# Performance work log

Hardware: AMD Instinct MI355X
Metric: run time of the kernel (lower is better)

The kernel has to match this reference:

```python
import jax, jax.numpy as jnp
import numpy as np

B, T, C, H = 4, 2048, 768, 64

def setup_inputs() -> dict:
    key = jax.random.key(0)
    kx, kq, kk, kv = jax.random.split(key, 4)
    x = jax.random.normal(kx, (B, T, C), dtype=jnp.float32)
    # torch Linear(C->H, bias=False): y = x @ W with W [C, H]
    s = 1.0 / np.sqrt(C)
    Wq = jax.random.normal(kq, (C, H), dtype=jnp.float32) * s
    Wk = jax.random.normal(kk, (C, H), dtype=jnp.float32) * s
    Wv = jax.random.normal(kv, (C, H), dtype=jnp.float32) * s
    return {"x": x, "Wq": Wq, "Wk": Wk, "Wv": Wv}

def reference(x, Wq, Wk, Wv):
    Bx, Tx, Cx = x.shape
    q = jnp.einsum('btc,ch->bth', x, Wq)
    k = jnp.einsum('btc,ch->bth', x, Wk)
    v = jnp.einsum('btc,ch->bth', x, Wv)
    # NOTE: original scales by C**-0.5 (n_embeddings), not head_size**-0.5
    w = jnp.einsum('bqh,bkh->bqk', q, k) * (Cx ** -0.5)  # [B, T, T]
    causal = jnp.tril(jnp.ones((Tx, Tx), dtype=bool))
    w = jnp.where(causal, w, -jnp.inf)
    w = jax.nn.softmax(w, axis=-1)
    # dropout: eval mode (identity)
    out = jnp.einsum('bqk,bkh->bqh', w, v)  # [B, T, H]
    return out
```

## Files before the change

### kernel.cpp

```cpp
#include <hip/hip_runtime.h>
#include <math.h>

#define TB 2048
#define CB 768
#define NB 4
#define NROWS (NB * TB)
#define NSMAX 16
#define WGPB 272

typedef __attribute__((ext_vector_type(8))) short bf16x8;
typedef __attribute__((ext_vector_type(4))) float f32x4;
typedef __attribute__((ext_vector_type(2))) float f32x2;
typedef __attribute__((ext_vector_type(2))) unsigned int u32x2;
typedef __attribute__((ext_vector_type(4))) unsigned int u32x4;

__device__ inline unsigned short f2bf(float f) {
  union { float f; unsigned u; } v; v.f = f;
  unsigned r = v.u + 0x7FFFu + ((v.u >> 16) & 1u);
  return (unsigned short)(r >> 16);
}
__device__ inline unsigned pack2bf(float a, float b) {
  return (unsigned)f2bf(a) | ((unsigned)f2bf(b) << 16);
}
__device__ inline float bf2f(unsigned short u) {
  union { unsigned u; float f; } v; v.u = (unsigned)u << 16; return v.f;
}
__device__ inline int groupP(int g) {
  int m = g >> 1;
  return (g & 1) ? (m + 1) * (m + 1) : m * (m + 1);
}

__global__ void cvt_w_kernel(const float* __restrict__ Wq, const float* __restrict__ Wk,
                             const float* __restrict__ Wv, unsigned short* __restrict__ Wt) {
  __shared__ float tw[64][65];
  const float* W = (blockIdx.y == 0) ? Wq : (blockIdx.y == 1) ? Wk : Wv;
  const int c0 = blockIdx.x * 64;
  const int row = threadIdx.x >> 2, seg = threadIdx.x & 3;
#pragma unroll
  for (int i = 0; i < 4; ++i) {
    float4 f = *(const float4*)(W + (size_t)(c0 + row) * 64 + seg * 16 + i * 4);
    tw[row][seg * 16 + i * 4 + 0] = f.x;
    tw[row][seg * 16 + i * 4 + 1] = f.y;
    tw[row][seg * 16 + i * 4 + 2] = f.z;
    tw[row][seg * 16 + i * 4 + 3] = f.w;
  }
  __syncthreads();
  const int j = threadIdx.x >> 2, cq = threadIdx.x & 3;
  unsigned short* dst = Wt + (size_t)(blockIdx.y * 64 + j) * CB + c0 + cq * 16;
  u32x4 ua, ub;
#pragma unroll
  for (int i = 0; i < 4; ++i) ua[i] = pack2bf(tw[cq * 16 + 2 * i][j], tw[cq * 16 + 2 * i + 1][j]);
#pragma unroll
  for (int i = 0; i < 4; ++i) ub[i] = pack2bf(tw[cq * 16 + 8 + 2 * i][j], tw[cq * 16 + 9 + 2 * i][j]);
  *(u32x4*)dst = ua;
  *(u32x4*)(dst + 8) = ub;
}

__launch_bounds__(256)
__global__ void proj_direct_kernel(const float* __restrict__ x,
                                   const unsigned short* __restrict__ Wt,
                                   unsigned short* __restrict__ q,
                                   unsigned short* __restrict__ k,
                                   unsigned short* __restrict__ vT) {
  __shared__ __align__(16) unsigned short xs[16 * 64];
  __shared__ float tr[64][17];
  const int tid = threadIdx.x;
  const int wv = tid >> 6;
  const int l = tid & 63;
  const int lrow = l & 15, lg = l >> 4;
  const int m0 = blockIdx.x * 16;
  const int srow = tid >> 4;
  const int sq = tid & 15;
  const float* xp = x + (size_t)(m0 + srow) * CB + sq * 4;
  const int swz = (srow & 7) << 4;

  f32x4 acc[3];
#pragma unroll
  for (int n = 0; n < 3; ++n) acc[n] = (f32x4){0.f, 0.f, 0.f, 0.f};

  float4 f = *(const float4*)xp;
  for (int k0 = 0; k0 < CB; k0 += 64) {
    {
      u32x2 c;
      c.x = pack2bf(f.x, f.y);
      c.y = pack2bf(f.z, f.w);
      *(u32x2*)((char*)xs + srow * 128 + ((sq * 8) ^ swz)) = c;
    }
    if (k0 + 64 < CB) f = *(const float4*)(xp + k0 + 64);
    __syncthreads();

#pragma unroll
    for (int s = 0; s < 2; ++s) {
      bf16x8 af = *(const bf16x8*)((const char*)xs + lrow * 128 +
                                   ((s * 64 + lg * 16) ^ ((lrow & 7) << 4)));
#pragma unroll
      for (int nf = 0; nf < 3; ++nf) {
        int col = wv * 48 + nf * 16 + lrow;
        bf16x8 bfr = *(const bf16x8*)(Wt + (size_t)col * CB + k0 + s * 32 + lg * 8);
        acc[nf] = __builtin_amdgcn_mfma_f32_16x16x32_bf16(af, bfr, acc[nf], 0, 0, 0);
      }
    }
    __syncthreads();
  }

#pragma unroll
  for (int nf = 0; nf < 3; ++nf) {
    int j = wv * 48 + nf * 16 + lrow;
#pragma unroll
    for (int r = 0; r < 4; ++r) {
      int grow = m0 + lg * 4 + r;
      if (j < 64)       q[(size_t)grow * 64 + j] = f2bf(acc[nf][r]);
      else if (j < 128) k[(size_t)grow * 64 + (j - 64)] = f2bf(acc[nf][r]);
      else              tr[j - 128][lg * 4 + r] = acc[nf][r];
    }
  }
  __syncthreads();
  {
    const int b = m0 >> 11, t0 = m0 & (TB - 1);
    const int h = tid >> 2, tq = tid & 3;
    u32x2 pk;
    pk.x = pack2bf(tr[h][tq * 4 + 0], tr[h][tq * 4 + 1]);
    pk.y = pack2bf(tr[h][tq * 4 + 2], tr[h][tq * 4 + 3]);
    *(u32x2*)(vT + ((size_t)(b * 64 + h)) * TB + t0 + tq * 4) = pk;
  }
}

__launch_bounds__(256)
__global__ void attn_kernel(const unsigned short* __restrict__ q,
                            const unsigned short* __restrict__ k,
                            const unsigned short* __restrict__ vT,
                            unsigned short* __restrict__ PO, float* __restrict__ Mp,
                            float* __restrict__ Lp) {
  __shared__ __align__(16) char ksm[2][8192];
  __shared__ __align__(16) char vsm[2][8192];
  const int tid = threadIdx.x;
  const int wid = tid >> 6, l = tid & 63;
  const int lrow = l & 15, lg = l >> 4;
  const int b = blockIdx.y;
  const int w = blockIdx.x;

  int g = (int)(2.f * sqrtf((float)w));
  if (g > 31) g = 31;
  while (g < 31 && groupP(g + 1) <= w) ++g;
  while (g > 0 && groupP(g) > w) --g;
  const int b128 = w - groupP(g);
  const int s64a = 2 * b128, s64b = 2 * b128 + 1;
  const bool has1 = (s64b <= g);
  const int kv0a = s64a * 64, kv0b = s64b * 64;
  const int qrow = (4 * g + wid) * 16 + lrow;

  const unsigned short* qb = q + (size_t)b * TB * 64;
  const char* kbb = (const char*)(k + (size_t)b * TB * 64);
  const unsigned short* vb = vT + (size_t)b * 64 * TB;

  const int srow = tid >> 2;
  const int sc = (tid & 3) * 32;
  const int kswz_w = (srow & 7) << 4;
  const int vswz_w = (srow & 3) << 5;

  float4 ka0 = *(const float4*)(kbb + (size_t)kv0a * 128 + tid * 32);
  float4 ka1 = *(const float4*)(kbb + (size_t)kv0a * 128 + tid * 32 + 16);
  const char* vrowa = (const char*)(vb + (size_t)srow * TB + kv0a);
  float4 va0 = *(const float4*)(vrowa + sc);
  float4 va1 = *(const float4*)(vrowa + sc + 16);

  bf16x8 qf[2];
#pragma unroll
  for (int s = 0; s < 2; ++s)
    qf[s] = *(const bf16x8*)(qb + (size_t)qrow * 64 + s * 32 + lg * 8);

  *(float4*)(ksm[0] + srow * 128 + ((sc + 0) ^ kswz_w)) = ka0;
  *(float4*)(ksm[0] + srow * 128 + ((sc + 16) ^ kswz_w)) = ka1;
  *(float4*)(vsm[0] + srow * 128 + ((sc + 0) ^ vswz_w)) = va0;
  *(float4*)(vsm[0] + srow * 128 + ((sc + 16) ^ vswz_w)) = va1;

  if (has1) {
    float4 kb0 = *(const float4*)(kbb + (size_t)kv0b * 128 + tid * 32);
    float4 kb1 = *(const float4*)(kbb + (size_t)kv0b * 128 + tid * 32 + 16);
    const char* vrowb = (const char*)(vb + (size_t)srow * TB + kv0b);
    float4 vb0 = *(const float4*)(vrowb + sc);
    float4 vb1 = *(const float4*)(vrowb + sc + 16);
    *(float4*)(ksm[1] + srow * 128 + ((sc + 0) ^ kswz_w)) = kb0;
    *(float4*)(ksm[1] + srow * 128 + ((sc + 16) ^ kswz_w)) = kb1;
    *(float4*)(vsm[1] + srow * 128 + ((sc + 0) ^ vswz_w)) = vb0;
    *(float4*)(vsm[1] + srow * 128 + ((sc + 16) ^ vswz_w)) = vb1;
  }
  __syncthreads();

  const int kswz = (lrow & 7) << 4;
  const float scale = 0.03608439182435161f;

  f32x4 S0[4];
#pragma unroll
  for (int cf = 0; cf < 4; ++cf) S0[cf] = (f32x4){0.f, 0.f, 0.f, 0.f};
#pragma unroll
  for (int cf = 0; cf < 4; ++cf) {
    const char* kp = ksm[0] + (cf * 16 + lrow) * 128;
#pragma unroll
    for (int s = 0; s < 2; ++s) {
      bf16x8 kf = *(const bf16x8*)(kp + ((s * 64 + lg * 16) ^ kswz));
      S0[cf] = __builtin_amdgcn_mfma_f32_16x16x32_bf16(kf, qf[s], S0[cf], 0, 0, 0);
    }
  }
  float tmx = -INFINITY;
  {
    const bool msk = (s64a == g);
#pragma unroll
    for (int cf = 0; cf < 4; ++cf)
#pragma unroll
      for (int r = 0; r < 4; ++r) {
        float vv = S0[cf][r] * scale;
        if (msk) {
          int kvi = kv0a + cf * 16 + lg * 4 + r;
          vv = (kvi > qrow) ? -INFINITY : vv;
        }
        S0[cf][r] = vv;
        tmx = fmaxf(tmx, vv);
      }
  }
  f32x4 S1[4];
  if (has1) {
#pragma unroll
    for (int cf = 0; cf < 4; ++cf) S1[cf] = (f32x4){0.f, 0.f, 0.f, 0.f};
#pragma unroll
    for (int cf = 0; cf < 4; ++cf) {
      const char* kp = ksm[1] + (cf * 16 + lrow) * 128;
#pragma unroll
      for (int s = 0; s < 2; ++s) {
        bf16x8 kf = *(const bf16x8*)(kp + ((s * 64 + lg * 16) ^ kswz));
        S1[cf] = __builtin_amdgcn_mfma_f32_16x16x32_bf16(kf, qf[s], S1[cf], 0, 0, 0);
      }
    }
    const bool msk = (s64b == g);
#pragma unroll
    for (int cf = 0; cf < 4; ++cf)
#pragma unroll
      for (int r = 0; r < 4; ++r) {
        float vv = S1[cf][r] * scale;
        if (msk) {
          int kvi = kv0b + cf * 16 + lg * 4 + r;
          vv = (kvi > qrow) ? -INFINITY : vv;
        }
        S1[cf][r] = vv;
        tmx = fmaxf(tmx, vv);
      }
  }
  tmx = fmaxf(tmx, __shfl_xor(tmx, 16));
  tmx = fmaxf(tmx, __shfl_xor(tmx, 32));

  float lsl = 0.f;
  f32x4 o[4];
#pragma unroll
  for (int hf = 0; hf < 4; ++hf) o[hf] = (f32x4){0.f, 0.f, 0.f, 0.f};
  const int rswz = (lrow & 3) << 5;

  {
    float p[4][4];
#pragma unroll
    for (int cf = 0; cf < 4; ++cf)
#pragma unroll
      for (int r = 0; r < 4; ++r) {
        float pe = __expf(S0[cf][r] - tmx);
        p[cf][r] = pe;
        lsl += pe;
      }
    union { unsigned u[4]; bf16x8 v; } pbu[2];
#pragma unroll
    for (int s = 0; s < 2; ++s) {
      pbu[s].u[0] = pack2bf(p[2 * s][0], p[2 * s][1]);
      pbu[s].u[1] = pack2bf(p[2 * s][2], p[2 * s][3]);
      pbu[s].u[2] = pack2bf(p[2 * s + 1][0], p[2 * s + 1][1]);
      pbu[s].u[3] = pack2bf(p[2 * s + 1][2], p[2 * s + 1][3]);
    }
#pragma unroll
    for (int s = 0; s < 2; ++s)
#pragma unroll
      for (int hf = 0; hf < 4; ++hf) {
        int r = hf * 16 + lrow;
        int a1 = r * 128 + ((s * 64 + lg * 8) ^ rswz);
        u32x2 lo = *(const u32x2*)(vsm[0] + a1);
        u32x2 hi = *(const u32x2*)(vsm[0] + (a1 ^ 32));
        union { unsigned u[4]; bf16x8 v; } vfu;
        vfu.u[0] = lo.x; vfu.u[1] = lo.y; vfu.u[2] = hi.x; vfu.u[3] = hi.y;
        o[hf] = __builtin_amdgcn_mfma_f32_16x16x32_bf16(vfu.v, pbu[s].v, o[hf], 0, 0, 0);
      }
  }
  if (has1) {
    float p[4][4];
#pragma unroll
    for (int cf = 0; cf < 4; ++cf)
#pragma unroll
      for (int r = 0; r < 4; ++r) {
        float pe = __expf(S1[cf][r] - tmx);
        p[cf][r] = pe;
        lsl += pe;
      }
    union { unsigned u[4]; bf16x8 v; } pbu[2];
#pragma unroll
    for (int s = 0; s < 2; ++s) {
      pbu[s].u[0] = pack2bf(p[2 * s][0], p[2 * s][1]);
      pbu[s].u[1] = pack2bf(p[2 * s][2], p[2 * s][3]);
      pbu[s].u[2] = pack2bf(p[2 * s + 1][0], p[2 * s + 1][1]);
      pbu[s].u[3] = pack2bf(p[2 * s + 1][2], p[2 * s + 1][3]);
    }
#pragma unroll
    for (int s = 0; s < 2; ++s)
#pragma unroll
      for (int hf = 0; hf < 4; ++hf) {
        int r = hf * 16 + lrow;
        int a1 = r * 128 + ((s * 64 + lg * 8) ^ rswz);
        u32x2 lo = *(const u32x2*)(vsm[1] + a1);
        u32x2 hi = *(const u32x2*)(vsm[1] + (a1 ^ 32));
        union { unsigned u[4]; bf16x8 v; } vfu;
        vfu.u[0] = lo.x; vfu.u[1] = lo.y; vfu.u[2] = hi.x; vfu.u[3] = hi.y;
        o[hf] = __builtin_amdgcn_mfma_f32_16x16x32_bf16(vfu.v, pbu[s].v, o[hf], 0, 0, 0);
      }
  }

  float ls = lsl;
  ls += __shfl_xor(ls, 16);
  ls += __shfl_xor(ls, 32);

  size_t rowg = (size_t)b128 * NROWS + b * TB + qrow;
  unsigned short* pop = PO + rowg * 64 + lg * 4;
#pragma unroll
  for (int hf = 0; hf < 4; ++hf) {
    u32x2 pk;
    pk.x = pack2bf(o[hf][0], o[hf][1]);
    pk.y = pack2bf(o[hf][2], o[hf][3]);
    *(u32x2*)(pop + hf * 16) = pk;
  }
  if (lg == 0) {
    Mp[rowg] = tmx;
    Lp[rowg] = ls;
  }
}

__global__ void attn_reduce_kernel(const unsigned short* __restrict__ PO,
                                   const float* __restrict__ Mp,
                                   const float* __restrict__ Lp,
                                   float* __restrict__ out) {
  int id = blockIdx.x * 256 + threadIdx.x;
  if (id >= NROWS * 32) return;
  int row = id >> 5, h0 = (id & 31) * 2;
  int t = row & (TB - 1);
  int ns = (t >> 7) + 1;
  float M = -INFINITY;
#pragma unroll 4
  for (int s = 0; s < ns; ++s) M = fmaxf(M, Mp[(size_t)s * NROWS + row]);
  float L = 0.f, a0 = 0.f, a1 = 0.f;
#pragma unroll 4
  for (int s = 0; s < ns; ++s) {
    float w = __expf(Mp[(size_t)s * NROWS + row] - M);
    L += Lp[(size_t)s * NROWS + row] * w;
    unsigned pv = *(const unsigned*)(PO + ((size_t)s * NROWS + row) * 64 + h0);
    a0 += bf2f((unsigned short)(pv & 0xffff)) * w;
    a1 += bf2f((unsigned short)(pv >> 16)) * w;
  }
  float rL = 1.f / L;
  f32x2 r; r.x = a0 * rL; r.y = a1 * rL;
  *(f32x2*)(out + (size_t)row * 64 + h0) = r;
}

extern "C" void kernel_launch(void* const* d_in, const int* in_sizes, int n_in,
                              void* d_out, int out_size, void* d_ws, size_t ws_size,
                              hipStream_t stream) {
  const float* x  = (const float*)d_in[0];
  const float* Wq = (const float*)d_in[1];
  const float* Wk = (const float*)d_in[2];
  const float* Wv = (const float*)d_in[3];
  float* out = (float*)d_out;

  unsigned short* Wt = (unsigned short*)d_ws;
  unsigned short* qb = Wt + 192 * CB;
  unsigned short* kb = qb + (size_t)NROWS * 64;
  unsigned short* vT = kb + (size_t)NROWS * 64;
  char* scratch = (char*)(vT + (size_t)NROWS * 64);

  unsigned short* PO = (unsigned short*)scratch;
  float* Mp = (float*)(scratch + (size_t)NSMAX * NROWS * 64 * 2);
  float* Lp = Mp + (size_t)NSMAX * NROWS;

  hipLaunchKernelGGL(cvt_w_kernel, dim3(12, 3), dim3(256), 0, stream,
                     Wq, Wk, Wv, Wt);
  hipLaunchKernelGGL(proj_direct_kernel, dim3(NROWS / 16), dim3(256), 0, stream,
                     x, Wt, qb, kb, vT);
  hipLaunchKernelGGL(attn_kernel, dim3(WGPB, NB), dim3(256), 0, stream,
                     qb, kb, vT, PO, Mp, Lp);
  hipLaunchKernelGGL(attn_reduce_kernel, dim3((NROWS * 32) / 256), dim3(256), 0, stream,
                     PO, Mp, Lp, out);
}
```

Baseline: 51.07 us.

## Widen attention workgroups to 128 query rows over full 128-key tiles

The attention kernel now runs 512-thread workgroups of 8 waves, covering 128 query rows against one 128-key block. Blocks come from a triangular index over 128x128 tiles, which replaces the older 64-row grouping, and the grid is halved. Each K/V tile is loaded once and shared by twice as many query waves, cutting redundant global loads and workgroup count. In exchange, every thread always loads both 64-key halves. Diagonal tiles leave some waves masked or idle, and the larger blocks may lower occupancy.

```diff
diff --git a/kernel.cpp b/kernel.cpp
--- a/kernel.cpp
+++ b/kernel.cpp
@@ -6,7 +6,7 @@
 #define NB 4
 #define NROWS (NB * TB)
 #define NSMAX 16
-#define WGPB 272
+#define WGPB 136
 
 typedef __attribute__((ext_vector_type(8))) short bf16x8;
 typedef __attribute__((ext_vector_type(4))) float f32x4;
@@ -24,10 +24,6 @@
 }
 __device__ inline float bf2f(unsigned short u) {
   union { unsigned u; float f; } v; v.u = (unsigned)u << 16; return v.f;
-}
-__device__ inline int groupP(int g) {
-  int m = g >> 1;
-  return (g & 1) ? (m + 1) * (m + 1) : m * (m + 1);
 }
 
 __global__ void cvt_w_kernel(const float* __restrict__ Wq, const float* __restrict__ Wk,
@@ -125,7 +121,7 @@
   }
 }
 
-__launch_bounds__(256)
+__launch_bounds__(512)
 __global__ void attn_kernel(const unsigned short* __restrict__ q,
                             const unsigned short* __restrict__ k,
                             const unsigned short* __restrict__ vT,
@@ -139,56 +135,42 @@
   const int b = blockIdx.y;
   const int w = blockIdx.x;
 
-  int g = (int)(2.f * sqrtf((float)w));
-  if (g > 31) g = 31;
-  while (g < 31 && groupP(g + 1) <= w) ++g;
-  while (g > 0 && groupP(g) > w) --g;
-  const int b128 = w - groupP(g);
-  const int s64a = 2 * b128, s64b = 2 * b128 + 1;
-  const bool has1 = (s64b <= g);
-  const int kv0a = s64a * 64, kv0b = s64b * 64;
-  const int qrow = (4 * g + wid) * 16 + lrow;
+  int g = (int)((sqrtf((float)(8 * w + 1)) - 1.f) * 0.5f);
+  while ((g + 1) * (g + 2) / 2 <= w) ++g;
+  while (g * (g + 1) / 2 > w) --g;
+  const int b128 = w - g * (g + 1) / 2;
+  const int kv0a = b128 * 128, kv0b = kv0a + 64;
+  const int t = 8 * g + wid;
+  const int q0w = t * 16;
+  const int qrow = q0w + lrow;
 
   const unsigned short* qb = q + (size_t)b * TB * 64;
   const char* kbb = (const char*)(k + (size_t)b * TB * 64);
   const unsigned short* vb = vT + (size_t)b * 64 * TB;
 
-  const int srow = tid >> 2;
-  const int sc = (tid & 3) * 32;
+  const int srow = tid >> 3;
+  const int sc = (tid & 7) * 16;
   const int kswz_w = (srow & 7) << 4;
   const int vswz_w = (srow & 3) << 5;
-
-  float4 ka0 = *(const float4*)(kbb + (size_t)kv0a * 128 + tid * 32);
-  float4 ka1 = *(const float4*)(kbb + (size_t)kv0a * 128 + tid * 32 + 16);
-  const char* vrowa = (const char*)(vb + (size_t)srow * TB + kv0a);
-  float4 va0 = *(const float4*)(vrowa + sc);
-  float4 va1 = *(const float4*)(vrowa + sc + 16);
+  float4 ka = *(const float4*)(kbb + (size_t)kv0a * 128 + tid * 16);
+  float4 kb2 = *(const float4*)(kbb + (size_t)kv0b * 128 + tid * 16);
+  float4 va = *(const float4*)((const char*)(vb + (size_t)srow * TB + kv0a) + sc);
+  float4 vb2 = *(const float4*)((const char*)(vb + (size_t)srow * TB + kv0b) + sc);
 
   bf16x8 qf[2];
 #pragma unroll
   for (int s = 0; s < 2; ++s)
     qf[s] = *(const bf16x8*)(qb + (size_t)qrow * 64 + s * 32 + lg * 8);
 
-  *(float4*)(ksm[0] + srow * 128 + ((sc + 0) ^ kswz_w)) = ka0;
-  *(float4*)(ksm[0] + srow * 128 + ((sc + 16) ^ kswz_w)) = ka1;
-  *(float4*)(vsm[0] + srow * 128 + ((sc + 0) ^ vswz_w)) = va0;
-  *(float4*)(vsm[0] + srow * 128 + ((sc + 16) ^ vswz_w)) = va1;
-
-  if (has1) {
-    float4 kb0 = *(const float4*)(kbb + (size_t)kv0b * 128 + tid * 32);
-    float4 kb1 = *(const float4*)(kbb + (size_t)kv0b * 128 + tid * 32 + 16);
-    const char* vrowb = (const char*)(vb + (size_t)srow * TB + kv0b);
-    float4 vb0 = *(const float4*)(vrowb + sc);
-    float4 vb1 = *(const float4*)(vrowb + sc + 16);
-    *(float4*)(ksm[1] + srow * 128 + ((sc + 0) ^ kswz_w)) = kb0;
-    *(float4*)(ksm[1] + srow * 128 + ((sc + 16) ^ kswz_w)) = kb1;
-    *(float4*)(vsm[1] + srow * 128 + ((sc + 0) ^ vswz_w)) = vb0;
-    *(float4*)(vsm[1] + srow * 128 + ((sc + 16) ^ vswz_w)) = vb1;
-  }
+  *(float4*)(ksm[0] + srow * 128 + (sc ^ kswz_w)) = ka;
+  *(float4*)(ksm[1] + srow * 128 + (sc ^ kswz_w)) = kb2;
+  *(float4*)(vsm[0] + srow * 128 + (sc ^ vswz_w)) = va;
+  *(float4*)(vsm[1] + srow * 128 + (sc ^ vswz_w)) = vb2;
   __syncthreads();
 
   const int kswz = (lrow & 7) << 4;
   const float scale = 0.03608439182435161f;
+  const bool useb = (kv0b <= q0w + 15);
 
   f32x4 S0[4];
 #pragma unroll
@@ -204,7 +186,7 @@
   }
   float tmx = -INFINITY;
   {
-    const bool msk = (s64a == g);
+    const bool msk = (kv0a + 63 > q0w);
 #pragma unroll
     for (int cf = 0; cf < 4; ++cf)
 #pragma unroll
@@ -219,7 +201,7 @@
       }
   }
   f32x4 S1[4];
-  if (has1) {
+  if (useb) {
 #pragma unroll
     for (int cf = 0; cf < 4; ++cf) S1[cf] = (f32x4){0.f, 0.f, 0.f, 0.f};
 #pragma unroll
@@ -231,7 +213,7 @@
         S1[cf] = __builtin_amdgcn_mfma_f32_16x16x32_bf16(kf, qf[s], S1[cf], 0, 0, 0);
       }
     }
-    const bool msk = (s64b == g);
+    const bool msk = (kv0b + 63 > q0w);
 #pragma unroll
     for (int cf = 0; cf < 4; ++cf)
 #pragma unroll
@@ -285,7 +267,7 @@
         o[hf] = __builtin_amdgcn_mfma_f32_16x16x32_bf16(vfu.v, pbu[s].v, o[hf], 0, 0, 0);
       }
   }
-  if (has1) {
+  if (useb) {
     float p[4][4];
 #pragma unroll
     for (int cf = 0; cf < 4; ++cf)
@@ -385,7 +367,7 @@
                      Wq, Wk, Wv, Wt);
   hipLaunchKernelGGL(proj_direct_kernel, dim3(NROWS / 16), dim3(256), 0, stream,
                      x, Wt, qb, kb, vT);
-  hipLaunchKernelGGL(attn_kernel, dim3(WGPB, NB), dim3(256), 0, stream,
+  hipLaunchKernelGGL(attn_kernel, dim3(WGPB, NB), dim3(512), 0, stream,
                      qb, kb, vT, PO, Mp, Lp);
   hipLaunchKernelGGL(attn_reduce_kernel, dim3((NROWS * 32) / 256), dim3(256), 0, stream,
                      PO, Mp, Lp, out);
```

After: 50.92 us (median of 3 runs). No clear change (-0.3%).
